# Kernel optimization log

Hardware: AMD Instinct MI355X
Metric: run time of the kernel (lower is better)

The kernel has to match this reference:

```python
import jax, jax.numpy as jnp
import numpy as np

B, S, D, H, DH, DM = 2, 2048, 1024, 16, 64, 4096
EPS = 1e-5
IGNORE = -100000.0
INIT_RANGE = 0.02


def setup_inputs() -> dict:
    key = jax.random.key(0)
    ks = jax.random.split(key, 8)
    inp = {
        "resid_pre": jax.random.normal(ks[0], (B, S, D), jnp.float32),
        "ln1_w": jnp.ones((D,), jnp.float32),
        "ln1_b": jnp.zeros((D,), jnp.float32),
        "W_Q": jax.random.normal(ks[1], (H, D, DH), jnp.float32) * 0.05,
        "b_Q": jnp.zeros((H, DH), jnp.float32),
        "W_K": jax.random.normal(ks[2], (H, D, DH), jnp.float32) * 0.05,
        "b_K": jnp.zeros((H, DH), jnp.float32),
        "W_V": jax.random.normal(ks[3], (H, D, DH), jnp.float32) * 0.05,
        "b_V": jnp.zeros((H, DH), jnp.float32),
        "W_O": jax.random.normal(ks[4], (H, DH, D), jnp.float32) * 0.05,
        "b_O": jnp.zeros((D,), jnp.float32),
        "ln2_w": jnp.ones((D,), jnp.float32),
        "ln2_b": jnp.zeros((D,), jnp.float32),
        "W_in": jax.random.normal(ks[5], (D, DM), jnp.float32) * INIT_RANGE,
        "b_in": jnp.zeros((DM,), jnp.float32),
        "W_out": jax.random.normal(ks[6], (DM, D), jnp.float32) * INIT_RANGE,
        "b_out": jnp.zeros((D,), jnp.float32),
    }
    return inp


def _layernorm(x, w, b):
    mean = jnp.mean(x, axis=-1, keepdims=True)
    xc = x - mean
    var = jnp.mean(jnp.square(xc), axis=-1, keepdims=True)
    return xc / jnp.sqrt(var + EPS) * w + b


def _attention(x, W_Q, b_Q, W_K, b_K, W_V, b_V, W_O, b_O):
    q = jnp.einsum('bqd,hdm->bqhm', x, W_Q) + b_Q
    k = jnp.einsum('bkd,hdm->bkhm', x, W_K) + b_K
    scores = jnp.einsum('bqhd,bkhd->bhqk', q, k) / jnp.sqrt(jnp.float32(DH))
    s = x.shape[1]
    causal = jnp.tril(jnp.ones((s, s), bool))  # True = keep
    scores = jnp.where(causal, scores, IGNORE)
    pattern = jax.nn.softmax(scores, axis=-1)
    v = jnp.einsum('bkd,hdm->bkhm', x, W_V) + b_V
    z = jnp.einsum('bhqk,bkhd->bqhd', pattern, v)
    return jnp.einsum('bqhd,hdm->bqm', z, W_O) + b_O


def reference(resid_pre, ln1_w, ln1_b, W_Q, b_Q, W_K, b_K, W_V, b_V, W_O, b_O,
              ln2_w, ln2_b, W_in, b_in, W_out, b_out):
    # Pre-LN attention + residual (dropout disabled: inference mode)
    attn_out = _attention(_layernorm(resid_pre, ln1_w, ln1_b),
                          W_Q, b_Q, W_K, b_K, W_V, b_V, W_O, b_O)
    resid_mid = resid_pre + attn_out
    # Pre-LN MLP + residual; keras gelu default is exact (erf-based)
    h = _layernorm(resid_mid, ln2_w, ln2_b)
    pre = jnp.einsum('bpd,dm->bpm', h, W_in) + b_in
    post = jax.nn.gelu(pre, approximate=False)
    mlp_out = jnp.einsum('bpm,md->bpd', post, W_out) + b_out
    return resid_mid + mlp_out
```

## Files before the change

### kernel.cpp

```cpp
#include <hip/hip_runtime.h>
#include <math.h>

#define S_LEN   2048
#define D_MODEL 1024
#define N_HEADS 16
#define D_HEAD  64
#define D_MLP   4096
#define T_TOKENS 4096
#define QSCALE_F 0.18033688011112042f

typedef __attribute__((ext_vector_type(8))) short short8;
typedef __attribute__((ext_vector_type(4))) float f32x4;
typedef unsigned short ushort_t;
typedef unsigned long long u64;

__device__ __forceinline__ ushort_t f2bf(float x) {
    unsigned int u = __float_as_uint(x);
    return (ushort_t)((u + 0x7FFFu + ((u >> 16) & 1u)) >> 16);
}

__device__ __forceinline__ float gelu_exact(float x) {
    return 0.5f * x * (1.0f + erff(x * 0.7071067811865476f));
}

__device__ __forceinline__ void gld_lds16(const void* g, void* l) {
    __builtin_amdgcn_global_load_lds(
        (const __attribute__((address_space(1))) unsigned int*)g,
        (__attribute__((address_space(3))) unsigned int*)l, 16, 0, 0);
}

__global__ __launch_bounds__(256) void ln_kernel(const float* __restrict__ x,
                                                 const float* __restrict__ w,
                                                 const float* __restrict__ b,
                                                 ushort_t* __restrict__ out) {
    int t = blockIdx.x;
    int tid = threadIdx.x;
    const float* xp = x + (size_t)t * D_MODEL;
    float4 v = *(const float4*)(xp + tid * 4);
    float s  = v.x + v.y + v.z + v.w;
    float sq = v.x*v.x + v.y*v.y + v.z*v.z + v.w*v.w;
    for (int o = 32; o; o >>= 1) {
        s  += __shfl_down(s, o, 64);
        sq += __shfl_down(sq, o, 64);
    }
    __shared__ float ss[4], ssq[4];
    if ((tid & 63) == 0) { ss[tid >> 6] = s; ssq[tid >> 6] = sq; }
    __syncthreads();
    float S  = ss[0] + ss[1] + ss[2] + ss[3];
    float SQ = ssq[0] + ssq[1] + ssq[2] + ssq[3];
    float mean = S * (1.0f / D_MODEL);
    float var  = SQ * (1.0f / D_MODEL) - mean * mean;
    float rstd = rsqrtf(var + 1e-5f);
    float4 wv = *(const float4*)(w + tid * 4);
    float4 bv = *(const float4*)(b + tid * 4);
    float ox = (v.x - mean) * rstd * wv.x + bv.x;
    float oy = (v.y - mean) * rstd * wv.y + bv.y;
    float oz = (v.z - mean) * rstd * wv.z + bv.z;
    float ow = (v.w - mean) * rstd * wv.w + bv.w;
    u64 pack = (u64)f2bf(ox) | ((u64)f2bf(oy) << 16) | ((u64)f2bf(oz) << 32) | ((u64)f2bf(ow) << 48);
    *(u64*)(out + (size_t)t * D_MODEL + tid * 4) = pack;
}

__global__ __launch_bounds__(256) void transpose_f2b(const float* __restrict__ in,
                                                     long long inStride, int ldin,
                                                     ushort_t* __restrict__ out,
                                                     long long outStride, int ldout) {
    in  += (size_t)blockIdx.z * inStride;
    out += (size_t)blockIdx.z * outStride;
    __shared__ float t[32][33];
    int c0 = blockIdx.x * 32, r0 = blockIdx.y * 32;
    int tx = threadIdx.x, ty = threadIdx.y;
    #pragma unroll
    for (int i = 0; i < 32; i += 8)
        t[ty + i][tx] = in[(size_t)(r0 + ty + i) * ldin + c0 + tx];
    __syncthreads();
    #pragma unroll
    for (int i = 0; i < 32; i += 8)
        out[(size_t)(c0 + ty + i) * ldout + r0 + tx] = f2bf(t[tx][ty + i]);
}

__global__ __launch_bounds__(256) void tpose_b2b(const ushort_t* __restrict__ in,
                                                 ushort_t* __restrict__ out) {
    int pair = blockIdx.z;
    in  += (size_t)pair * (S_LEN * 64);
    out += (size_t)pair * (S_LEN * 64);
    __shared__ ushort_t t[32][33];
    int s0 = blockIdx.x * 32, d0 = blockIdx.y * 32;
    int tx = threadIdx.x, ty = threadIdx.y;
    #pragma unroll
    for (int i = 0; i < 32; i += 8)
        t[ty + i][tx] = in[(size_t)(s0 + ty + i) * 64 + d0 + tx];
    __syncthreads();
    #pragma unroll
    for (int i = 0; i < 32; i += 8)
        out[(size_t)(d0 + ty + i) * S_LEN + s0 + tx] = t[tx][ty + i];
}

__global__ __launch_bounds__(256) void qkv_bias_cat(const float* __restrict__ bq,
                                                    const float* __restrict__ bk,
                                                    const float* __restrict__ bv,
                                                    float* __restrict__ out) {
    int i = blockIdx.x * 256 + threadIdx.x;
    float v = (i < 1024) ? bq[i] : (i < 2048 ? bk[i - 1024] : bv[i - 2048]);
    out[i] = v;
}

template<int OUT_MODE, bool DO_GELU, bool HAS_RES>
__global__ __launch_bounds__(256, 4) void mfma_gemm(
    const ushort_t* __restrict__ A, int lda,
    const ushort_t* __restrict__ Bt, int ldb,
    void* __restrict__ Cv, int ldc, int K,
    const float* __restrict__ bias,
    const float* __restrict__ res, int ldres) {

    __shared__ ushort_t As[2][128 * 32];
    __shared__ ushort_t Bs[2][128 * 32];

    int tid  = threadIdx.x;
    int lane = tid & 63;
    int n0 = blockIdx.x * 128, m0 = blockIdx.y * 128;
    int wave = tid >> 6;
    int wm = (wave & 1) * 64, wn = (wave >> 1) * 64;
    int quad = lane >> 4, l15 = lane & 15;

    int srow = tid >> 2, skc = (tid & 3) * 8;
    const ushort_t* Ap  = A  + (size_t)(m0 + srow)      * lda + skc;
    const ushort_t* Ap2 = A  + (size_t)(m0 + srow + 64) * lda + skc;
    const ushort_t* Bp  = Bt + (size_t)(n0 + srow)      * ldb + skc;
    const ushort_t* Bp2 = Bt + (size_t)(n0 + srow + 64) * ldb + skc;

    f32x4 acc[4][4];
    #pragma unroll
    for (int i = 0; i < 4; ++i)
        #pragma unroll
        for (int j = 0; j < 4; ++j)
            acc[i][j] = (f32x4){0.f, 0.f, 0.f, 0.f};

    gld_lds16(Ap,       &As[0][tid * 8]);
    gld_lds16(Ap2,      &As[0][(tid + 256) * 8]);
    gld_lds16(Bp,       &Bs[0][tid * 8]);
    gld_lds16(Bp2,      &Bs[0][(tid + 256) * 8]);

    int niter = K >> 5;
    for (int j = 0; j < niter; ++j) {
        __syncthreads();
        int p = j & 1;
        if (j + 1 < niter) {
            int k1 = (j + 1) << 5;
            gld_lds16(Ap  + k1, &As[p ^ 1][tid * 8]);
            gld_lds16(Ap2 + k1, &As[p ^ 1][(tid + 256) * 8]);
            gld_lds16(Bp  + k1, &Bs[p ^ 1][tid * 8]);
            gld_lds16(Bp2 + k1, &Bs[p ^ 1][(tid + 256) * 8]);
        }
        short8 a[4], b[4];
        #pragma unroll
        for (int i = 0; i < 4; ++i) {
            a[i] = *(const short8*)&As[p][(wm + i * 16 + l15) * 32 + quad * 8];
            b[i] = *(const short8*)&Bs[p][(wn + i * 16 + l15) * 32 + quad * 8];
        }
        #pragma unroll
        for (int i = 0; i < 4; ++i)
            #pragma unroll
            for (int jj = 0; jj < 4; ++jj)
                acc[i][jj] = __builtin_amdgcn_mfma_f32_16x16x32_bf16(a[i], b[jj], acc[i][jj], 0, 0, 0);
    }

    #pragma unroll
    for (int i = 0; i < 4; ++i) {
        int rBase = m0 + wm + i * 16 + quad * 4;
        #pragma unroll
        for (int j = 0; j < 4; ++j) {
            int col = n0 + wn + j * 16 + l15;
            float bv = bias ? bias[col] : 0.f;
            #pragma unroll
            for (int r = 0; r < 4; ++r) {
                int rowg = rBase + r;
                float v = acc[i][j][r] + bv;
                if (DO_GELU) v = gelu_exact(v);
                if (HAS_RES) v += res[(size_t)rowg * ldres + col];
                if (OUT_MODE == 0)
                    ((float*)Cv)[(size_t)rowg * ldc + col] = v;
                else
                    ((ushort_t*)Cv)[(size_t)rowg * ldc + col] = f2bf(v);
            }
        }
    }
}

__global__ __launch_bounds__(256, 4) void mfma_gemm_qkv(
    const ushort_t* __restrict__ A, const ushort_t* __restrict__ Bt,
    ushort_t* __restrict__ Qh, ushort_t* __restrict__ Kh, ushort_t* __restrict__ Vh,
    const float* __restrict__ bias) {

    const int lda = 1024, ldb = 1024, K = 1024;
    __shared__ ushort_t As[2][128 * 32];
    __shared__ ushort_t Bs[2][128 * 32];

    int tid  = threadIdx.x;
    int lane = tid & 63;
    int n0 = blockIdx.x * 128, m0 = blockIdx.y * 128;
    int wave = tid >> 6;
    int wm = (wave & 1) * 64, wn = (wave >> 1) * 64;
    int quad = lane >> 4, l15 = lane & 15;

    int srow = tid >> 2, skc = (tid & 3) * 8;
    const ushort_t* Ap  = A  + (size_t)(m0 + srow)      * lda + skc;
    const ushort_t* Ap2 = A  + (size_t)(m0 + srow + 64) * lda + skc;
    const ushort_t* Bp  = Bt + (size_t)(n0 + srow)      * ldb + skc;
    const ushort_t* Bp2 = Bt + (size_t)(n0 + srow + 64) * ldb + skc;

    f32x4 acc[4][4];
    #pragma unroll
    for (int i = 0; i < 4; ++i)
        #pragma unroll
        for (int j = 0; j < 4; ++j)
            acc[i][j] = (f32x4){0.f, 0.f, 0.f, 0.f};

    gld_lds16(Ap,  &As[0][tid * 8]);
    gld_lds16(Ap2, &As[0][(tid + 256) * 8]);
    gld_lds16(Bp,  &Bs[0][tid * 8]);
    gld_lds16(Bp2, &Bs[0][(tid + 256) * 8]);

    const int niter = K >> 5;
    for (int j = 0; j < niter; ++j) {
        __syncthreads();
        int p = j & 1;
        if (j + 1 < niter) {
            int k1 = (j + 1) << 5;
            gld_lds16(Ap  + k1, &As[p ^ 1][tid * 8]);
            gld_lds16(Ap2 + k1, &As[p ^ 1][(tid + 256) * 8]);
            gld_lds16(Bp  + k1, &Bs[p ^ 1][tid * 8]);
            gld_lds16(Bp2 + k1, &Bs[p ^ 1][(tid + 256) * 8]);
        }
        short8 a[4], b[4];
        #pragma unroll
        for (int i = 0; i < 4; ++i) {
            a[i] = *(const short8*)&As[p][(wm + i * 16 + l15) * 32 + quad * 8];
            b[i] = *(const short8*)&Bs[p][(wn + i * 16 + l15) * 32 + quad * 8];
        }
        #pragma unroll
        for (int i = 0; i < 4; ++i)
            #pragma unroll
            for (int jj = 0; jj < 4; ++jj)
                acc[i][jj] = __builtin_amdgcn_mfma_f32_16x16x32_bf16(a[i], b[jj], acc[i][jj], 0, 0, 0);
    }

    #pragma unroll
    for (int i = 0; i < 4; ++i) {
        int rBase = m0 + wm + i * 16 + quad * 4;
        #pragma unroll
        for (int j = 0; j < 4; ++j) {
            int col = n0 + wn + j * 16 + l15;
            int sel = col >> 10;
            int h   = (col >> 6) & 15;
            int dh  = col & 63;
            ushort_t* dst = (sel == 0) ? Qh : (sel == 1 ? Kh : Vh);
            float sc = (sel == 0) ? QSCALE_F : 1.0f;
            float bv = bias[col];
            #pragma unroll
            for (int r = 0; r < 4; ++r) {
                int rowg = rBase + r;
                int bb = rowg >> 11, s = rowg & 2047;
                float v = (acc[i][j][r] + bv) * sc;
                dst[((size_t)(bb * 16 + h) * S_LEN + s) * 64 + dh] = f2bf(v);
            }
        }
    }
}

__global__ __launch_bounds__(256, 4) void flash_kernel(
    const ushort_t* __restrict__ Qh, const ushort_t* __restrict__ Kh,
    const ushort_t* __restrict__ Vt, ushort_t* __restrict__ Z) {

    __shared__ ushort_t Klds[2][64 * 64];
    __shared__ ushort_t Vlds[2][64 * 64];
    __shared__ ushort_t Plds[4][16 * 64];

    int pair = blockIdx.x;
    int qt   = blockIdx.y;
    int q0   = qt * 64;
    int tid = threadIdx.x, lane = tid & 63, wave = tid >> 6;
    int quad = lane >> 4, l15 = lane & 15;

    const ushort_t* Qbase = Qh + (size_t)pair * (S_LEN * 64);
    const ushort_t* Kbase = Kh + (size_t)pair * (S_LEN * 64);
    const ushort_t* Vbase = Vt + (size_t)pair * (S_LEN * 64);
    ushort_t* Qstage = &Plds[0][0];

    #pragma unroll
    for (int n = 0; n < 2; ++n) {
        int c = tid + n * 256;
        int row = c >> 3, part = c & 7;
        gld_lds16(Qbase + (size_t)(q0 + row) * 64 + ((part ^ (row & 7)) * 8), Qstage + c * 8);
    }
    __syncthreads();
    short8 qa[2];
    #pragma unroll
    for (int h = 0; h < 2; ++h) {
        int row = wave * 16 + l15;
        int part = (h * 4 + quad) ^ (row & 7);
        qa[h] = *(const short8*)(Qstage + row * 64 + part * 8);
    }

    f32x4 ls = (f32x4){0.f, 0.f, 0.f, 0.f};
    f32x4 zacc[4];
    #pragma unroll
    for (int dht = 0; dht < 4; ++dht) zacc[dht] = (f32x4){0.f, 0.f, 0.f, 0.f};

    #pragma unroll
    for (int n = 0; n < 2; ++n) {
        int c = tid + n * 256;
        int row = c >> 3, part = c & 7;
        int gp = (part ^ (row & 7)) * 8;
        gld_lds16(Kbase + (size_t)row * 64 + gp, &Klds[0][0] + c * 8);
        gld_lds16(Vbase + (size_t)row * S_LEN + gp, &Vlds[0][0] + c * 8);
    }

    for (int j = 0; j <= qt; ++j) {
        __syncthreads();
        int p = j & 1;
        if (j < qt) {
            int k1 = (j + 1) * 64;
            #pragma unroll
            for (int n = 0; n < 2; ++n) {
                int c = tid + n * 256;
                int row = c >> 3, part = c & 7;
                int gp = (part ^ (row & 7)) * 8;
                gld_lds16(Kbase + (size_t)(k1 + row) * 64 + gp, &Klds[p ^ 1][0] + c * 8);
                gld_lds16(Vbase + (size_t)row * S_LEN + k1 + gp, &Vlds[p ^ 1][0] + c * 8);
            }
        }
        const ushort_t* Kc = &Klds[p][0];
        const ushort_t* Vc = &Vlds[p][0];

        f32x4 s[4];
        #pragma unroll
        for (int jt = 0; jt < 4; ++jt) {
            int krow = jt * 16 + l15;
            int sw = krow & 7;
            short8 kb0 = *(const short8*)(Kc + krow * 64 + ((quad ^ sw) * 8));
            short8 kb1 = *(const short8*)(Kc + krow * 64 + (((quad + 4) ^ sw) * 8));
            f32x4 t = __builtin_amdgcn_mfma_f32_16x16x32_bf16(qa[0], kb0,
                        (f32x4){0.f, 0.f, 0.f, 0.f}, 0, 0, 0);
            s[jt] = __builtin_amdgcn_mfma_f32_16x16x32_bf16(qa[1], kb1, t, 0, 0, 0);
        }

        if (j == qt) {
            #pragma unroll
            for (int jt = 0; jt < 4; ++jt) {
                int kc = jt * 16 + l15;
                int qr = wave * 16 + quad * 4;
                #pragma unroll
                for (int r = 0; r < 4; ++r)
                    if (kc > qr + r) s[jt][r] = -1e30f;
            }
        }

        #pragma unroll
        for (int jt = 0; jt < 4; ++jt) {
            #pragma unroll
            for (int r = 0; r < 4; ++r) {
                float pv = exp2f(s[jt][r]);
                s[jt][r] = pv;
                ls[r] += pv;
            }
        }

        ushort_t* Pw = &Plds[wave][0];
        #pragma unroll
        for (int jt = 0; jt < 4; ++jt) {
            int col = jt * 16 + l15;
            int cp = col >> 3, ci = col & 7;
            #pragma unroll
            for (int r = 0; r < 4; ++r) {
                int prow = quad * 4 + r;
                Pw[prow * 64 + ((cp ^ (prow & 7)) * 8) + ci] = f2bf(s[jt][r]);
            }
        }

        #pragma unroll
        for (int kc = 0; kc < 2; ++kc) {
            int prow = l15;
            short8 pa = *(const short8*)(Pw + prow * 64 + ((((kc * 4 + quad) ^ (prow & 7))) * 8));
            #pragma unroll
            for (int dht = 0; dht < 4; ++dht) {
                int vrow = dht * 16 + l15;
                short8 vb = *(const short8*)(Vc + vrow * 64 + ((((kc * 4 + quad) ^ (vrow & 7))) * 8));
                zacc[dht] = __builtin_amdgcn_mfma_f32_16x16x32_bf16(pa, vb, zacc[dht], 0, 0, 0);
            }
        }
    }

    #pragma unroll
    for (int d = 1; d < 16; d <<= 1) {
        ls[0] += __shfl_xor(ls[0], d, 64);
        ls[1] += __shfl_xor(ls[1], d, 64);
        ls[2] += __shfl_xor(ls[2], d, 64);
        ls[3] += __shfl_xor(ls[3], d, 64);
    }
    int bb = pair >> 4, h = pair & 15;
    #pragma unroll
    for (int r = 0; r < 4; ++r) {
        int qrow = q0 + wave * 16 + quad * 4 + r;
        size_t tok = (size_t)bb * S_LEN + qrow;
        float inv = 1.0f / ls[r];
        #pragma unroll
        for (int dht = 0; dht < 4; ++dht)
            Z[tok * D_MODEL + h * 64 + dht * 16 + l15] = f2bf(zacc[dht][r] * inv);
    }
}

extern "C" void kernel_launch(void* const* d_in, const int* in_sizes, int n_in,
                              void* d_out, int out_size, void* d_ws, size_t ws_size,
                              hipStream_t stream) {
    const float* resid_pre = (const float*)d_in[0];
    const float* ln1_w = (const float*)d_in[1];
    const float* ln1_b = (const float*)d_in[2];
    const float* W_Q   = (const float*)d_in[3];
    const float* b_Q   = (const float*)d_in[4];
    const float* W_K   = (const float*)d_in[5];
    const float* b_K   = (const float*)d_in[6];
    const float* W_V   = (const float*)d_in[7];
    const float* b_V   = (const float*)d_in[8];
    const float* W_O   = (const float*)d_in[9];
    const float* b_O   = (const float*)d_in[10];
    const float* ln2_w = (const float*)d_in[11];
    const float* ln2_b = (const float*)d_in[12];
    const float* W_in  = (const float*)d_in[13];
    const float* b_in  = (const float*)d_in[14];
    const float* W_out = (const float*)d_in[15];
    const float* b_out = (const float*)d_in[16];
    float* out = (float*)d_out;
    char* W = (char*)d_ws;

    const size_t MB = 1u << 20;
    ushort_t* Qh     = (ushort_t*)(W + 0 * MB);
    ushort_t* Kh     = (ushort_t*)(W + 8 * MB);
    ushort_t* Vh     = (ushort_t*)(W + 16 * MB);
    ushort_t* Vt     = (ushort_t*)(W + 24 * MB);
    ushort_t* Zbf    = (ushort_t*)(W + 32 * MB);
    ushort_t* LN1a   = (ushort_t*)(W + 40 * MB);
    ushort_t* Wqkv   = (ushort_t*)(W + 48 * MB);
    ushort_t* Wo_t   = (ushort_t*)(W + 54 * MB);
    ushort_t* Win_t  = (ushort_t*)(W + 56 * MB);
    ushort_t* Wout_t = (ushort_t*)(W + 64 * MB);
    ushort_t* LN2a   = (ushort_t*)(W + 72 * MB);
    ushort_t* MLPh   = (ushort_t*)(W + 80 * MB);
    float*    MID    = (float*)  (W + 112 * MB);
    float*    qbias  = (float*)  (W + 128 * MB);

    const size_t M1 = 1u << 20;
    dim3 tb(32, 8);

    transpose_f2b<<<dim3(2, 32, 16), tb, 0, stream>>>(W_Q, 65536, 64, Wqkv,          65536, 1024);
    transpose_f2b<<<dim3(2, 32, 16), tb, 0, stream>>>(W_K, 65536, 64, Wqkv + 1 * M1, 65536, 1024);
    transpose_f2b<<<dim3(2, 32, 16), tb, 0, stream>>>(W_V, 65536, 64, Wqkv + 2 * M1, 65536, 1024);
    qkv_bias_cat<<<12, 256, 0, stream>>>(b_Q, b_K, b_V, qbias);
    ln_kernel<<<T_TOKENS, 256, 0, stream>>>(resid_pre, ln1_w, ln1_b, LN1a);

    mfma_gemm_qkv<<<dim3(24, 32), 256, 0, stream>>>(LN1a, Wqkv, Qh, Kh, Vh, qbias);
    tpose_b2b<<<dim3(64, 2, 32), tb, 0, stream>>>(Vh, Vt);

    flash_kernel<<<dim3(32, 32), 256, 0, stream>>>(Qh, Kh, Vt, Zbf);

    transpose_f2b<<<dim3(32, 32, 1), tb, 0, stream>>>(W_O, 0, 1024, Wo_t, 0, 1024);
    mfma_gemm<0, false, true><<<dim3(8, 32), 256, 0, stream>>>(
        Zbf, 1024, Wo_t, 1024, MID, 1024, 1024, b_O, resid_pre, 1024);

    ln_kernel<<<T_TOKENS, 256, 0, stream>>>(MID, ln2_w, ln2_b, LN2a);
    transpose_f2b<<<dim3(128, 32, 1), tb, 0, stream>>>(W_in,  0, 4096, Win_t,  0, 1024);
    transpose_f2b<<<dim3(32, 128, 1), tb, 0, stream>>>(W_out, 0, 1024, Wout_t, 0, 4096);
    mfma_gemm<1, true, false><<<dim3(32, 32), 256, 0, stream>>>(
        LN2a, 1024, Win_t, 1024, MLPh, 4096, 1024, b_in, nullptr, 0);
    mfma_gemm<0, false, true><<<dim3(8, 32), 256, 0, stream>>>(
        MLPh, 4096, Wout_t, 4096, out, 1024, 4096, b_out, MID, 1024);
}
```

Baseline: 405.7 us.

## Split K across two wave groups in the narrow output GEMMs

Adds a 512-thread GEMM variant in which two groups of four waves each process half of the K dimension into separate LDS double buffers. Group 1 then writes its partial accumulators to shared memory, and group 0 adds them before the bias and residual epilogue. It is applied to the attention output projection and the MLP down projection, which launch only 256 blocks with 256 threads each. The aim is to put more waves on each CU for these small grids, at the cost of a 64KB LDS footprint, an extra LDS reduction and lower block occupancy.

Measured after the change: 384.2 us. 5.3% less time.

```diff
diff --git a/kernel.cpp b/kernel.cpp
--- a/kernel.cpp
+++ b/kernel.cpp
@@ -136,10 +136,10 @@
         for (int j = 0; j < 4; ++j)
             acc[i][j] = (f32x4){0.f, 0.f, 0.f, 0.f};
 
-    gld_lds16(Ap,       &As[0][tid * 8]);
-    gld_lds16(Ap2,      &As[0][(tid + 256) * 8]);
-    gld_lds16(Bp,       &Bs[0][tid * 8]);
-    gld_lds16(Bp2,      &Bs[0][(tid + 256) * 8]);
+    gld_lds16(Ap,  &As[0][tid * 8]);
+    gld_lds16(Ap2, &As[0][(tid + 256) * 8]);
+    gld_lds16(Bp,  &Bs[0][tid * 8]);
+    gld_lds16(Bp2, &Bs[0][(tid + 256) * 8]);
 
     int niter = K >> 5;
     for (int j = 0; j < niter; ++j) {
@@ -185,6 +185,109 @@
             }
         }
     }
+}
+
+template<int OUT_MODE, bool DO_GELU, bool HAS_RES>
+__global__ __launch_bounds__(512, 2) void mfma_gemm_sk(
+    const ushort_t* __restrict__ A, int lda,
+    const ushort_t* __restrict__ Bt, int ldb,
+    void* __restrict__ Cv, int ldc, int K,
+    const float* __restrict__ bias,
+    const float* __restrict__ res, int ldres) {
+
+    __shared__ ushort_t Smem[32768];
+    #define SA_(g, p) (Smem + ((g) * 2 + (p)) * 4096)
+    #define SB_(g, p) (Smem + 16384 + ((g) * 2 + (p)) * 4096)
+
+    int tid  = threadIdx.x;
+    int lane = tid & 63;
+    int wave = tid >> 6;
+    int g = wave >> 2, w = wave & 3;
+    int n0 = blockIdx.x * 128, m0 = blockIdx.y * 128;
+    int wm = (w & 1) * 64, wn = (w >> 1) * 64;
+    int quad = lane >> 4, l15 = lane & 15;
+
+    int lt = tid & 255;
+    int srow = lt >> 2, skc = (lt & 3) * 8;
+    int kbase = g * (K >> 1);
+    const ushort_t* Ap  = A  + (size_t)(m0 + srow)      * lda + kbase + skc;
+    const ushort_t* Ap2 = A  + (size_t)(m0 + srow + 64) * lda + kbase + skc;
+    const ushort_t* Bp  = Bt + (size_t)(n0 + srow)      * ldb + kbase + skc;
+    const ushort_t* Bp2 = Bt + (size_t)(n0 + srow + 64) * ldb + kbase + skc;
+
+    f32x4 acc[4][4];
+    #pragma unroll
+    for (int i = 0; i < 4; ++i)
+        #pragma unroll
+        for (int j = 0; j < 4; ++j)
+            acc[i][j] = (f32x4){0.f, 0.f, 0.f, 0.f};
+
+    gld_lds16(Ap,  SA_(g, 0) + lt * 8);
+    gld_lds16(Ap2, SA_(g, 0) + (lt + 256) * 8);
+    gld_lds16(Bp,  SB_(g, 0) + lt * 8);
+    gld_lds16(Bp2, SB_(g, 0) + (lt + 256) * 8);
+
+    int niter = K >> 6;
+    for (int j = 0; j < niter; ++j) {
+        __syncthreads();
+        int p = j & 1;
+        if (j + 1 < niter) {
+            int k1 = (j + 1) << 5;
+            gld_lds16(Ap  + k1, SA_(g, p ^ 1) + lt * 8);
+            gld_lds16(Ap2 + k1, SA_(g, p ^ 1) + (lt + 256) * 8);
+            gld_lds16(Bp  + k1, SB_(g, p ^ 1) + lt * 8);
+            gld_lds16(Bp2 + k1, SB_(g, p ^ 1) + (lt + 256) * 8);
+        }
+        const ushort_t* Ac = SA_(g, p);
+        const ushort_t* Bc = SB_(g, p);
+        short8 a[4], b[4];
+        #pragma unroll
+        for (int i = 0; i < 4; ++i) {
+            a[i] = *(const short8*)(Ac + (wm + i * 16 + l15) * 32 + quad * 8);
+            b[i] = *(const short8*)(Bc + (wn + i * 16 + l15) * 32 + quad * 8);
+        }
+        #pragma unroll
+        for (int i = 0; i < 4; ++i)
+            #pragma unroll
+            for (int jj = 0; jj < 4; ++jj)
+                acc[i][jj] = __builtin_amdgcn_mfma_f32_16x16x32_bf16(a[i], b[jj], acc[i][jj], 0, 0, 0);
+    }
+
+    __syncthreads();
+    float* R = (float*)Smem;
+    if (g == 1) {
+        #pragma unroll
+        for (int i = 0; i < 4; ++i)
+            #pragma unroll
+            for (int j = 0; j < 4; ++j)
+                *(f32x4*)&R[(((w * 16 + i * 4 + j) * 64) + lane) * 4] = acc[i][j];
+    }
+    __syncthreads();
+    if (g == 0) {
+        #pragma unroll
+        for (int i = 0; i < 4; ++i) {
+            int rBase = m0 + wm + i * 16 + quad * 4;
+            #pragma unroll
+            for (int j = 0; j < 4; ++j) {
+                f32x4 other = *(const f32x4*)&R[(((w * 16 + i * 4 + j) * 64) + lane) * 4];
+                int col = n0 + wn + j * 16 + l15;
+                float bv = bias ? bias[col] : 0.f;
+                #pragma unroll
+                for (int r = 0; r < 4; ++r) {
+                    int rowg = rBase + r;
+                    float v = acc[i][j][r] + other[r] + bv;
+                    if (DO_GELU) v = gelu_exact(v);
+                    if (HAS_RES) v += res[(size_t)rowg * ldres + col];
+                    if (OUT_MODE == 0)
+                        ((float*)Cv)[(size_t)rowg * ldc + col] = v;
+                    else
+                        ((ushort_t*)Cv)[(size_t)rowg * ldc + col] = f2bf(v);
+                }
+            }
+        }
+    }
+    #undef SA_
+    #undef SB_
 }
 
 __global__ __launch_bounds__(256, 4) void mfma_gemm_qkv(
@@ -464,7 +567,7 @@
     flash_kernel<<<dim3(32, 32), 256, 0, stream>>>(Qh, Kh, Vt, Zbf);
 
     transpose_f2b<<<dim3(32, 32, 1), tb, 0, stream>>>(W_O, 0, 1024, Wo_t, 0, 1024);
-    mfma_gemm<0, false, true><<<dim3(8, 32), 256, 0, stream>>>(
+    mfma_gemm_sk<0, false, true><<<dim3(8, 32), 512, 0, stream>>>(
         Zbf, 1024, Wo_t, 1024, MID, 1024, 1024, b_O, resid_pre, 1024);
 
     ln_kernel<<<T_TOKENS, 256, 0, stream>>>(MID, ln2_w, ln2_b, LN2a);
@@ -472,6 +575,6 @@
     transpose_f2b<<<dim3(32, 128, 1), tb, 0, stream>>>(W_out, 0, 1024, Wout_t, 0, 4096);
     mfma_gemm<1, true, false><<<dim3(32, 32), 256, 0, stream>>>(
         LN2a, 1024, Win_t, 1024, MLPh, 4096, 1024, b_in, nullptr, 0);
-    mfma_gemm<0, false, true><<<dim3(8, 32), 256, 0, stream>>>(
+    mfma_gemm_sk<0, false, true><<<dim3(8, 32), 512, 0, stream>>>(
         MLPh, 4096, Wout_t, 4096, out, 1024, 4096, b_out, MID, 1024);
 }
```
